# Kernel tuning notes

Hardware: AMD Instinct MI355X
Metric: run time of the kernel (lower is better)

## Reference

```python
import jax, jax.numpy as jnp
import numpy as np

T = 4096        # tokens
D = 1024        # input_dim
H = 2048        # expert_hidden_dim
O = 1024        # output_dim
E = 8           # num_experts
K = 2           # top_k


def setup_inputs() -> dict:
    key = jax.random.key(0)
    ks = jax.random.split(key, 7)
    s_in = 1.0 / np.sqrt(D)
    s_h = 1.0 / np.sqrt(H)
    return {
        "x": jax.random.normal(ks[0], (T, D), dtype=jnp.float32),
        "Wg": jax.random.uniform(ks[1], (D, E), jnp.float32, -s_in, s_in),
        "bg": jax.random.uniform(ks[2], (E,), jnp.float32, -s_in, s_in),
        "W1": jax.random.uniform(ks[3], (E, D, H), jnp.float32, -s_in, s_in),
        "b1": jax.random.uniform(ks[4], (E, H), jnp.float32, -s_in, s_in),
        "W2": jax.random.uniform(ks[5], (E, H, O), jnp.float32, -s_h, s_h),
        "b2": jax.random.uniform(ks[6], (E, O), jnp.float32, -s_h, s_h),
    }


def reference(x, Wg, bg, W1, b1, W2, b2):
    # Gating: top-k over expert logits, softmax over the k selected logits.
    logits = x @ Wg + bg                                  # [T, E]
    top_vals, top_idx = jax.lax.top_k(logits, K)          # [T, K]
    gates = jax.nn.softmax(top_vals, axis=-1)             # [T, K]

    # Expert MLPs (Linear -> ReLU -> Linear). Each token is processed by the
    # experts it routes to; since an expert's output on x is route-independent,
    # compute all expert outputs once and gather the selected ones (static
    # shapes, jit-friendly equivalent of the masked dispatch loop).
    h = jax.nn.relu(jnp.einsum('td,edh->eth', x, W1) + b1[:, None, :])  # [E,T,H]
    y = jnp.einsum('eth,eho->eto', h, W2) + b2[:, None, :]              # [E,T,O]

    sel = y[top_idx, jnp.arange(T)[:, None]]              # [T, K, O]
    # Weighted combine (scatter_add over batch_idx == per-token sum over K).
    return jnp.sum(sel * gates[..., None], axis=1)        # [T, O]
```

## Files before the change

kernel.cpp:

```cpp
#include <hip/hip_runtime.h>
#include <math.h>


#define T_TOK 4096
#define DIM   1024
#define HID   2048
#define OUTD  1024
#define NE    8

typedef __bf16 bf16_t;
typedef __bf16 bf16x8 __attribute__((ext_vector_type(8)));
typedef float  f32x4  __attribute__((ext_vector_type(4)));

typedef __attribute__((address_space(3))) void       as3_void;
typedef __attribute__((address_space(1))) const void as1_void;
#define GLDS16(src, dst) \
  __builtin_amdgcn_global_load_lds((as1_void*)(src), (as3_void*)(dst), 16, 0, 0)

#define FENCE() asm volatile("" ::: "memory")
#define BARRIER() do { FENCE(); __builtin_amdgcn_s_barrier(); FENCE(); } while (0)
#define LGKM_WAIT() do { \
    asm volatile("s_waitcnt lgkmcnt(0)" ::: "memory"); \
    __builtin_amdgcn_sched_barrier(0); } while (0)
#define VMW_RING() do { \
    if (wid < 4) asm volatile("s_waitcnt vmcnt(4)" ::: "memory"); \
    else         asm volatile("s_waitcnt vmcnt(3)" ::: "memory"); } while (0)
#define VM_WAIT0() asm volatile("s_waitcnt vmcnt(0)" ::: "memory")

__device__ __forceinline__ void gate_body(int bid, const float* __restrict__ x,
                                          const float* __restrict__ Wg,
                                          const float* __restrict__ bg,
                                          int* __restrict__ einfo,
                                          float2* __restrict__ gpair,
                                          bf16_t* __restrict__ xb) {
  int wid  = threadIdx.x >> 6;
  int lane = threadIdx.x & 63;
  int t = bid * 4 + wid;

  const float4* xr = (const float4*)(x + (size_t)t * DIM);
  float4 xv4[4];
  float sf[NE];
#pragma unroll
  for (int e = 0; e < NE; ++e) sf[e] = 0.f;

#pragma unroll
  for (int i = 0; i < 4; ++i) {
    int q = lane + 64 * i;
    float4 xv = xr[q];
    xv4[i] = xv;
    int d = q * 4;
#pragma unroll
    for (int c = 0; c < 4; ++c) {
      float xc = (&xv.x)[c];
      const float4* wr = (const float4*)(Wg + (size_t)(d + c) * NE);
      float4 w0 = wr[0], w1 = wr[1];
      sf[0] += xc * w0.x; sf[1] += xc * w0.y;
      sf[2] += xc * w0.z; sf[3] += xc * w0.w;
      sf[4] += xc * w1.x; sf[5] += xc * w1.y;
      sf[6] += xc * w1.z; sf[7] += xc * w1.w;
    }
  }

  ushort4* xbr = (ushort4*)(xb + (size_t)t * DIM);
#pragma unroll
  for (int i = 0; i < 4; ++i) {
    union { bf16_t b[4]; ushort4 u; } cv;
    cv.b[0] = (bf16_t)xv4[i].x; cv.b[1] = (bf16_t)xv4[i].y;
    cv.b[2] = (bf16_t)xv4[i].z; cv.b[3] = (bf16_t)xv4[i].w;
    xbr[lane + 64 * i] = cv.u;
  }

  double s[NE];
#pragma unroll
  for (int e = 0; e < NE; ++e) s[e] = (double)sf[e];
#pragma unroll
  for (int off = 32; off > 0; off >>= 1) {
#pragma unroll
    for (int e = 0; e < NE; ++e) s[e] += __shfl_xor(s[e], off);
  }

  if (lane == 0) {
    double v0 = -1e300, v1 = -1e300;
    int i0 = 0, i1 = 0;
#pragma unroll
    for (int e = 0; e < NE; ++e) {
      double v = s[e] + (double)bg[e];
      if (v > v0)      { v1 = v0; i1 = i0; v0 = v; i0 = e; }
      else if (v > v1) { v1 = v;  i1 = e; }
    }
    float ex = expf((float)(v1 - v0));
    float inv = 1.0f / (1.0f + ex);
    einfo[t] = i0 | (i1 << 8);
    gpair[t] = make_float2(inv, ex * inv);
  }
}

__device__ __forceinline__ void tr_body(const float* __restrict__ W,
                                        bf16_t* __restrict__ Wt, int R, int C,
                                        int bx, int by, int e, char* lds) {
  size_t ebase = (size_t)e * R * C;
  const int r0 = by * 64, c0 = bx * 128;
  const int tid = threadIdx.x;
#pragma unroll
  for (int it = 0; it < 8; ++it) {
    int f = tid + 256 * it;
    int row = f >> 5, cq = f & 31;
    float4 v = *(const float4*)&W[ebase + (size_t)(r0 + row) * C + c0 + cq * 4];
    union { bf16_t b[4]; unsigned long long u; } cv;
    cv.b[0] = (bf16_t)v.x; cv.b[1] = (bf16_t)v.y;
    cv.b[2] = (bf16_t)v.z; cv.b[3] = (bf16_t)v.w;
    *(unsigned long long*)(lds + row * 256 + ((cq ^ (row & 31)) << 3)) = cv.u;
  }
  __syncthreads();
#pragma unroll
  for (int p = 0; p < 4; ++p) {
    int q = tid + 256 * p;
    int orow = q >> 3, j = q & 7;
    union { bf16_t b[8]; uint4 u; } cv;
#pragma unroll
    for (int i = 0; i < 8; ++i) {
      int r = j * 8 + i;
      cv.b[i] = *(const bf16_t*)(lds + r * 256 +
                                 ((((orow >> 2) ^ (r & 31)) << 3) +
                                  ((orow & 3) << 1)));
    }
    *(uint4*)&Wt[ebase + (size_t)(c0 + orow) * R + r0 + j * 8] = cv.u;
  }
}

#define NB_GATE (T_TOK / 4)
#define NB_TR1  ((DIM / 64) * (HID / 128) * NE)
#define NB_TR2  ((HID / 64) * (OUTD / 128) * NE)
__global__ void k_front(const float* __restrict__ x, const float* __restrict__ Wg,
                        const float* __restrict__ bg, int* __restrict__ einfo,
                        float2* __restrict__ gpair, bf16_t* __restrict__ xb,
                        const float* __restrict__ W1, bf16_t* __restrict__ W1t,
                        const float* __restrict__ W2, bf16_t* __restrict__ W2t) {
  __shared__ __align__(16) char lds[16384];
  int bid = blockIdx.x;
  if (bid < NB_GATE) {
    gate_body(bid, x, Wg, bg, einfo, gpair, xb);
  } else if (bid < NB_GATE + NB_TR1) {
    int i = bid - NB_GATE;
    int nbx = HID / 128, nby = DIM / 64;
    tr_body(W1, W1t, DIM, HID, i % nbx, (i / nbx) % nby, i / (nbx * nby), lds);
  } else {
    int i = bid - NB_GATE - NB_TR1;
    int nbx = OUTD / 128, nby = HID / 64;
    tr_body(W2, W2t, HID, OUTD, i % nbx, (i / nbx) % nby, i / (nbx * nby), lds);
  }
}

__global__ void k_bin(const int* __restrict__ einfo, const float2* __restrict__ gpair,
                      int* __restrict__ cnt, int* __restrict__ offs,
                      int* __restrict__ elist, float* __restrict__ egate,
                      int* __restrict__ tokrec) {
  __shared__ int scnt[NE];
  int w = threadIdx.x >> 6;
  int lane = threadIdx.x & 63;
  unsigned long long below = (lane == 0) ? 0ull : ((~0ull) >> (64 - lane));
  int base = 0;
  for (int c = 0; c < T_TOK / 64; ++c) {
    int t = c * 64 + lane;
    int ei = einfo[t];
    float2 g = gpair[t];
    int e0 = ei & 0xff, e1 = ei >> 8;
    bool m0 = (e0 == w);
    bool m  = m0 || (e1 == w);
    unsigned long long mask = __ballot(m);
    if (m) {
      int pos = base + (int)__popcll(mask & below);
      elist[w * T_TOK + pos] = t;
      egate[w * T_TOK + pos] = m0 ? g.x : g.y;
      tokrec[2 * t + (m0 ? 0 : 1)] = (w << 16) | pos;
    }
    base += (int)__popcll(mask);
  }
  if (lane == 0) scnt[w] = base;
  __syncthreads();
  if (threadIdx.x == 0) {
    int a = 0;
#pragma unroll
    for (int e = 0; e < NE; ++e) {
      cnt[e] = scnt[e];
      offs[e] = a;
      a += scnt[e];
    }
    offs[NE] = a;
  }
}

#define STAGE_A(TT, HH) do { \
    char* _d = smem + (((TT) & 1) * 24576) + ((HH) * 12288); \
    GLDS16(Abase + offA[HH][0] + (TT) * 128, _d + tid * 16); \
    if (tid < 256) GLDS16(Abase + offA[HH][1] + (TT) * 128, _d + (512 + tid) * 16); \
  } while (0)

#define STAGE_B(TT, HH) do { \
    char* _d = smem + 49152 + (((TT) & 1) * 32768) + ((HH) * 16384); \
    GLDS16(Bbase + offB[HH][0] + (TT) * 128, _d + tid * 16); \
    GLDS16(Bbase + offB[HH][1] + (TT) * 128, _d + (512 + tid) * 16); \
  } while (0)

#define MFMA_Q(AF, BF, AH, BH) \
    _Pragma("unroll") for (int i = 0; i < 3; ++i) \
      _Pragma("unroll") for (int j = 0; j < 2; ++j) \
        _Pragma("unroll") for (int kk = 0; kk < 2; ++kk) \
          acc[(AH) * 3 + i][(BH) * 2 + j] = \
            __builtin_amdgcn_mfma_f32_16x16x32_bf16(AF[i][kk], BF[j][kk], \
                acc[(AH) * 3 + i][(BH) * 2 + j], 0, 0, 0)

#define RD_AF(SL) \
    _Pragma("unroll") for (int i = 0; i < 3; ++i) \
      _Pragma("unroll") for (int kk = 0; kk < 2; ++kk) \
        af[i][kk] = *(const bf16x8*)((SL) + rdA[i][kk])

#define KTILE(TT, NTc) do { \
    const char* _a0 = smem + (((TT) & 1) * 24576); \
    const char* _a1 = smem + (((TT) & 1) * 24576) + 12288; \
    const char* _b0 = smem + 49152 + (((TT) & 1) * 32768); \
    const char* _b1 = smem + 49152 + (((TT) & 1) * 32768) + 16384; \
    bf16x8 af[3][2], bf0[2][2], bf1[2][2]; \
    RD_AF(_a0); \
    _Pragma("unroll") for (int j = 0; j < 2; ++j) \
      _Pragma("unroll") for (int kk = 0; kk < 2; ++kk) { \
        bf0[j][kk] = *(const bf16x8*)(_b0 + rdB[j][kk]); \
        bf1[j][kk] = *(const bf16x8*)(_b1 + rdB[j][kk]); \
      } \
    if ((TT) + 1 < (NTc)) { STAGE_A((TT) + 1, 1); STAGE_B((TT) + 1, 1); } \
    BARRIER(); LGKM_WAIT(); \
    __builtin_amdgcn_s_setprio(1); \
    MFMA_Q(af, bf0, 0, 0); MFMA_Q(af, bf1, 0, 1); \
    __builtin_amdgcn_s_setprio(0); BARRIER(); \
    RD_AF(_a1); \
    if ((TT) + 2 < (NTc)) { STAGE_A((TT) + 2, 0); STAGE_B((TT) + 2, 0); \
      VMW_RING(); } \
    else { VM_WAIT0(); } \
    BARRIER(); LGKM_WAIT(); \
    __builtin_amdgcn_s_setprio(1); \
    MFMA_Q(af, bf0, 1, 0); MFMA_Q(af, bf1, 1, 1); \
    __builtin_amdgcn_s_setprio(0); BARRIER(); \
  } while (0)

__launch_bounds__(512, 2)
__global__ void k_gemm1(const bf16_t* __restrict__ xb, const bf16_t* __restrict__ W1t,
                        const float* __restrict__ b1, const int* __restrict__ cnt,
                        const int* __restrict__ offs, const int* __restrict__ elist,
                        bf16_t* __restrict__ hbuf) {
  const int e = blockIdx.z;
  const int count = cnt[e];
  const int rt = blockIdx.y;
  if (rt * 192 >= count) return;
  const int nt = blockIdx.x;

  __shared__ __align__(16) char smem[114688];

  const int tid = threadIdx.x, lane = tid & 63, wid = tid >> 6;
  const int wm = wid >> 2, wn = wid & 3;
  const int fr = lane & 15, lh = lane >> 4;

  unsigned offA[2][2], offB[2][2];
#pragma unroll
  for (int j = 0; j < 2; ++j) {
    int q = j * 512 + tid;
    int r = q >> 3, sfg = (q & 7) ^ (r & 7);
#pragma unroll
    for (int h = 0; h < 2; ++h) {
      int ar = r < 96 ? r : 95;
      int gr = rt * 192 + h * 96 + ar;
      if (gr > count - 1) gr = count - 1;
      int tok = elist[e * T_TOK + gr];
      offA[h][j] = (unsigned)((tok * DIM + sfg * 8) * 2);
      int brow = nt * 256 + h * 128 + r;
      offB[h][j] = (unsigned)(((e * HID + brow) * DIM + sfg * 8) * 2);
    }
  }
  unsigned rdA[3][2], rdB[2][2];
#pragma unroll
  for (int i = 0; i < 3; ++i) {
    int r = wm * 48 + i * 16 + fr;
#pragma unroll
    for (int kk = 0; kk < 2; ++kk)
      rdA[i][kk] = (unsigned)(r * 128 + (((kk * 4 + lh) ^ (r & 7)) * 16));
  }
#pragma unroll
  for (int j = 0; j < 2; ++j) {
    int r = wn * 32 + j * 16 + fr;
#pragma unroll
    for (int kk = 0; kk < 2; ++kk)
      rdB[j][kk] = (unsigned)(r * 128 + (((kk * 4 + lh) ^ (r & 7)) * 16));
  }

  const char* Abase = (const char*)xb;
  const char* Bbase = (const char*)W1t;

  f32x4 acc[6][4];
#pragma unroll
  for (int i = 0; i < 6; ++i)
#pragma unroll
    for (int j = 0; j < 4; ++j) acc[i][j] = (f32x4){0.f, 0.f, 0.f, 0.f};

  const int NT = DIM / 64;
  STAGE_A(0, 0); STAGE_B(0, 0); STAGE_A(0, 1); STAGE_B(0, 1);
  STAGE_A(1, 0); STAGE_B(1, 0);
  VMW_RING();
  BARRIER();

  for (int t = 0; t < NT; ++t) KTILE(t, NT);

  const int hbase = offs[e];
#pragma unroll
  for (int mi = 0; mi < 6; ++mi) {
#pragma unroll
    for (int rr = 0; rr < 4; ++rr) {
      int rowp = rt * 192 + (mi / 3) * 96 + wm * 48 + (mi % 3) * 16 + lh * 4 + rr;
      if (rowp < count) {
        size_t hrow = (size_t)(hbase + rowp) * HID;
#pragma unroll
        for (int nj = 0; nj < 4; ++nj) {
          int col = nt * 256 + (nj >> 1) * 128 + wn * 32 + (nj & 1) * 16 + fr;
          float v = acc[mi][nj][rr] + b1[e * HID + col];
          hbuf[hrow + col] = (bf16_t)(v > 0.f ? v : 0.f);
        }
      }
    }
  }
}

__launch_bounds__(512, 2)
__global__ void k_gemm2(const bf16_t* __restrict__ hbuf, const bf16_t* __restrict__ W2t,
                        const float* __restrict__ b2, const int* __restrict__ cnt,
                        const int* __restrict__ offs, const float* __restrict__ egate,
                        float* __restrict__ y) {
  const int e = blockIdx.z;
  const int count = cnt[e];
  const int rt = blockIdx.y;
  if (rt * 192 >= count) return;
  const int nt = blockIdx.x;

  __shared__ __align__(16) char smem[114688];

  const int tid = threadIdx.x, lane = tid & 63, wid = tid >> 6;
  const int wm = wid >> 2, wn = wid & 3;
  const int fr = lane & 15, lh = lane >> 4;
  const int hbase = offs[e];

  unsigned offA[2][2], offB[2][2];
#pragma unroll
  for (int j = 0; j < 2; ++j) {
    int q = j * 512 + tid;
    int r = q >> 3, sfg = (q & 7) ^ (r & 7);
#pragma unroll
    for (int h = 0; h < 2; ++h) {
      int ar = r < 96 ? r : 95;
      int gr = rt * 192 + h * 96 + ar;
      if (gr > count - 1) gr = count - 1;
      offA[h][j] = (unsigned)(((hbase + gr) * HID + sfg * 8) * 2);
      int brow = nt * 256 + h * 128 + r;
      offB[h][j] = (unsigned)(((e * OUTD + brow) * HID + sfg * 8) * 2);
    }
  }
  unsigned rdA[3][2], rdB[2][2];
#pragma unroll
  for (int i = 0; i < 3; ++i) {
    int r = wm * 48 + i * 16 + fr;
#pragma unroll
    for (int kk = 0; kk < 2; ++kk)
      rdA[i][kk] = (unsigned)(r * 128 + (((kk * 4 + lh) ^ (r & 7)) * 16));
  }
#pragma unroll
  for (int j = 0; j < 2; ++j) {
    int r = wn * 32 + j * 16 + fr;
#pragma unroll
    for (int kk = 0; kk < 2; ++kk)
      rdB[j][kk] = (unsigned)(r * 128 + (((kk * 4 + lh) ^ (r & 7)) * 16));
  }

  const char* Abase = (const char*)hbuf;
  const char* Bbase = (const char*)W2t;

  f32x4 acc[6][4];
#pragma unroll
  for (int i = 0; i < 6; ++i)
#pragma unroll
    for (int j = 0; j < 4; ++j) acc[i][j] = (f32x4){0.f, 0.f, 0.f, 0.f};

  const int NT = HID / 64;
  STAGE_A(0, 0); STAGE_B(0, 0); STAGE_A(0, 1); STAGE_B(0, 1);
  STAGE_A(1, 0); STAGE_B(1, 0);
  VMW_RING();
  BARRIER();

  for (int t = 0; t < NT; ++t) KTILE(t, NT);

#pragma unroll
  for (int mi = 0; mi < 6; ++mi) {
#pragma unroll
    for (int rr = 0; rr < 4; ++rr) {
      int rowp = rt * 192 + (mi / 3) * 96 + wm * 48 + (mi % 3) * 16 + lh * 4 + rr;
      if (rowp < count) {
        float gate = egate[e * T_TOK + rowp];
        size_t yrow = (size_t)(hbase + rowp) * OUTD;
#pragma unroll
        for (int nj = 0; nj < 4; ++nj) {
          int col = nt * 256 + (nj >> 1) * 128 + wn * 32 + (nj & 1) * 16 + fr;
          y[yrow + col] = gate * (acc[mi][nj][rr] + b2[e * OUTD + col]);
        }
      }
    }
  }
}

__global__ void k_combine(const float* __restrict__ y, const int* __restrict__ offs,
                          const int* __restrict__ tokrec, float* __restrict__ out) {
  int t = blockIdx.x;
  int r0 = tokrec[2 * t], r1 = tokrec[2 * t + 1];
  int s0 = offs[r0 >> 16] + (r0 & 0xffff);
  int s1 = offs[r1 >> 16] + (r1 & 0xffff);
  const float4* ya = (const float4*)(y + (size_t)s0 * OUTD);
  const float4* yb = (const float4*)(y + (size_t)s1 * OUTD);
  float4* o = (float4*)(out + (size_t)t * OUTD);
  int i = threadIdx.x;
  float4 a = ya[i], b = yb[i];
  o[i] = make_float4(a.x + b.x, a.y + b.y, a.z + b.z, a.w + b.w);
}

extern "C" void kernel_launch(void* const* d_in, const int* in_sizes, int n_in,
                              void* d_out, int out_size, void* d_ws, size_t ws_size,
                              hipStream_t stream) {
  const float* x  = (const float*)d_in[0];
  const float* Wg = (const float*)d_in[1];
  const float* bg = (const float*)d_in[2];
  const float* W1 = (const float*)d_in[3];
  const float* b1 = (const float*)d_in[4];
  const float* W2 = (const float*)d_in[5];
  const float* b2 = (const float*)d_in[6];
  float* out = (float*)d_out;

  char* ws = (char*)d_ws;
  int*    cnt    = (int*)(ws);
  int*    offs   = (int*)(ws + 1024);
  int*    tokrec = (int*)(ws + 4096);
  int*    einfo  = (int*)(ws + 36864);
  float2* gpair  = (float2*)(ws + 53248);
  int*    elist  = (int*)(ws + 131072);
  float*  egate  = (float*)(ws + 262144);
  bf16_t* W1t    = (bf16_t*)(ws + (1u << 20));
  float*  y      = (float*)(ws + (1u << 20));
  bf16_t* W2t    = (bf16_t*)(ws + (1u << 20) + (32u << 20));
  bf16_t* xb     = (bf16_t*)(ws + (1u << 20) + (64u << 20));
  bf16_t* hbuf   = (bf16_t*)(ws + (1u << 20) + (72u << 20));

  k_front<<<NB_GATE + NB_TR1 + NB_TR2, 256, 0, stream>>>(
      x, Wg, bg, einfo, gpair, xb, W1, W1t, W2, W2t);
  k_bin<<<1, 512, 0, stream>>>(einfo, gpair, cnt, offs, elist, egate, tokrec);

  k_gemm1<<<dim3(HID / 256, 22, NE), 512, 0, stream>>>(
      xb, W1t, b1, cnt, offs, elist, hbuf);
  k_gemm2<<<dim3(OUTD / 256, 22, NE), 512, 0, stream>>>(
      hbuf, W2t, b2, cnt, offs, egate, y);
  k_combine<<<T_TOK, 256, 0, stream>>>(y, offs, tokrec, out);
}
```

Measured before the change: 200.5 us.

## Move W2 transpose-convert into extra gemm1 grid slice to overlap with GEMM

The fp32-to-bf16 transpose of W2 is removed from the front kernel and performed by an extra z-slice of the gemm1 grid (176 blocks, each handling two tiles per iteration with split LDS halves). The aim is to shorten the front kernel and overlap the W2 conversion with the first expert GEMM, filling CUs left idle by early-exiting row tiles. The cost is that these conversion blocks compete with gemm1 blocks for CU slots, memory bandwidth and a large LDS allocation. tr_body also gains an extra barrier.

```diff
diff --git a/kernel.cpp b/kernel.cpp
--- a/kernel.cpp
+++ b/kernel.cpp
@@ -97,57 +97,57 @@
 
 __device__ __forceinline__ void tr_body(const float* __restrict__ W,
                                         bf16_t* __restrict__ Wt, int R, int C,
-                                        int bx, int by, int e, char* lds) {
+                                        int bx, int by, int e, char* lds,
+                                        int tid, bool valid) {
   size_t ebase = (size_t)e * R * C;
   const int r0 = by * 64, c0 = bx * 128;
-  const int tid = threadIdx.x;
-#pragma unroll
-  for (int it = 0; it < 8; ++it) {
-    int f = tid + 256 * it;
-    int row = f >> 5, cq = f & 31;
-    float4 v = *(const float4*)&W[ebase + (size_t)(r0 + row) * C + c0 + cq * 4];
-    union { bf16_t b[4]; unsigned long long u; } cv;
-    cv.b[0] = (bf16_t)v.x; cv.b[1] = (bf16_t)v.y;
-    cv.b[2] = (bf16_t)v.z; cv.b[3] = (bf16_t)v.w;
-    *(unsigned long long*)(lds + row * 256 + ((cq ^ (row & 31)) << 3)) = cv.u;
+  if (valid) {
+#pragma unroll
+    for (int it = 0; it < 8; ++it) {
+      int f = tid + 256 * it;
+      int row = f >> 5, cq = f & 31;
+      float4 v = *(const float4*)&W[ebase + (size_t)(r0 + row) * C + c0 + cq * 4];
+      union { bf16_t b[4]; unsigned long long u; } cv;
+      cv.b[0] = (bf16_t)v.x; cv.b[1] = (bf16_t)v.y;
+      cv.b[2] = (bf16_t)v.z; cv.b[3] = (bf16_t)v.w;
+      *(unsigned long long*)(lds + row * 256 + ((cq ^ (row & 31)) << 3)) = cv.u;
+    }
   }
   __syncthreads();
-#pragma unroll
-  for (int p = 0; p < 4; ++p) {
-    int q = tid + 256 * p;
-    int orow = q >> 3, j = q & 7;
-    union { bf16_t b[8]; uint4 u; } cv;
-#pragma unroll
-    for (int i = 0; i < 8; ++i) {
-      int r = j * 8 + i;
-      cv.b[i] = *(const bf16_t*)(lds + r * 256 +
-                                 ((((orow >> 2) ^ (r & 31)) << 3) +
-                                  ((orow & 3) << 1)));
-    }
-    *(uint4*)&Wt[ebase + (size_t)(c0 + orow) * R + r0 + j * 8] = cv.u;
-  }
+  if (valid) {
+#pragma unroll
+    for (int p = 0; p < 4; ++p) {
+      int q = tid + 256 * p;
+      int orow = q >> 3, j = q & 7;
+      union { bf16_t b[8]; uint4 u; } cv;
+#pragma unroll
+      for (int i = 0; i < 8; ++i) {
+        int r = j * 8 + i;
+        cv.b[i] = *(const bf16_t*)(lds + r * 256 +
+                                   ((((orow >> 2) ^ (r & 31)) << 3) +
+                                    ((orow & 3) << 1)));
+      }
+      *(uint4*)&Wt[ebase + (size_t)(c0 + orow) * R + r0 + j * 8] = cv.u;
+    }
+  }
+  __syncthreads();
 }
 
 #define NB_GATE (T_TOK / 4)
 #define NB_TR1  ((DIM / 64) * (HID / 128) * NE)
-#define NB_TR2  ((HID / 64) * (OUTD / 128) * NE)
 __global__ void k_front(const float* __restrict__ x, const float* __restrict__ Wg,
                         const float* __restrict__ bg, int* __restrict__ einfo,
                         float2* __restrict__ gpair, bf16_t* __restrict__ xb,
-                        const float* __restrict__ W1, bf16_t* __restrict__ W1t,
-                        const float* __restrict__ W2, bf16_t* __restrict__ W2t) {
+                        const float* __restrict__ W1, bf16_t* __restrict__ W1t) {
   __shared__ __align__(16) char lds[16384];
   int bid = blockIdx.x;
   if (bid < NB_GATE) {
     gate_body(bid, x, Wg, bg, einfo, gpair, xb);
-  } else if (bid < NB_GATE + NB_TR1) {
+  } else {
     int i = bid - NB_GATE;
     int nbx = HID / 128, nby = DIM / 64;
-    tr_body(W1, W1t, DIM, HID, i % nbx, (i / nbx) % nby, i / (nbx * nby), lds);
-  } else {
-    int i = bid - NB_GATE - NB_TR1;
-    int nbx = OUTD / 128, nby = HID / 64;
-    tr_body(W2, W2t, HID, OUTD, i % nbx, (i / nbx) % nby, i / (nbx * nby), lds);
+    tr_body(W1, W1t, DIM, HID, i % nbx, (i / nbx) % nby, i / (nbx * nby),
+            lds, threadIdx.x, true);
   }
 }
 
@@ -246,16 +246,35 @@
 __global__ void k_gemm1(const bf16_t* __restrict__ xb, const bf16_t* __restrict__ W1t,
                         const float* __restrict__ b1, const int* __restrict__ cnt,
                         const int* __restrict__ offs, const int* __restrict__ elist,
-                        bf16_t* __restrict__ hbuf) {
+                        bf16_t* __restrict__ hbuf,
+                        const float* __restrict__ W2, bf16_t* __restrict__ W2t) {
+  __shared__ __align__(16) char smem[114688];
+  const int tid = threadIdx.x;
+
+  if (blockIdx.z == NE) {
+    int bid2 = blockIdx.y * (HID / 256) + blockIdx.x;
+    char* lds2 = smem + ((tid >= 256) ? 16384 : 0);
+    int ltid = tid & 255;
+    const int NTILE = (HID / 64) * (OUTD / 128) * NE;
+    int nbx = OUTD / 128, nby = HID / 64;
+    for (int it = 0; it < 6; ++it) {
+      int tile = it * 352 + bid2 * 2 + (tid >= 256 ? 1 : 0);
+      bool valid = tile < NTILE;
+      int bx = valid ? tile % nbx : 0;
+      int by = valid ? (tile / nbx) % nby : 0;
+      int e2 = valid ? tile / (nbx * nby) : 0;
+      tr_body(W2, W2t, HID, OUTD, bx, by, e2, lds2, ltid, valid);
+    }
+    return;
+  }
+
   const int e = blockIdx.z;
   const int count = cnt[e];
   const int rt = blockIdx.y;
   if (rt * 192 >= count) return;
   const int nt = blockIdx.x;
 
-  __shared__ __align__(16) char smem[114688];
-
-  const int tid = threadIdx.x, lane = tid & 63, wid = tid >> 6;
+  const int lane = tid & 63, wid = tid >> 6;
   const int wm = wid >> 2, wn = wid & 3;
   const int fr = lane & 15, lh = lane >> 4;
 
@@ -451,12 +470,12 @@
   bf16_t* xb     = (bf16_t*)(ws + (1u << 20) + (64u << 20));
   bf16_t* hbuf   = (bf16_t*)(ws + (1u << 20) + (72u << 20));
 
-  k_front<<<NB_GATE + NB_TR1 + NB_TR2, 256, 0, stream>>>(
-      x, Wg, bg, einfo, gpair, xb, W1, W1t, W2, W2t);
+  k_front<<<NB_GATE + NB_TR1, 256, 0, stream>>>(
+      x, Wg, bg, einfo, gpair, xb, W1, W1t);
   k_bin<<<1, 512, 0, stream>>>(einfo, gpair, cnt, offs, elist, egate, tokrec);
 
-  k_gemm1<<<dim3(HID / 256, 22, NE), 512, 0, stream>>>(
-      xb, W1t, b1, cnt, offs, elist, hbuf);
+  k_gemm1<<<dim3(HID / 256, 22, NE + 1), 512, 0, stream>>>(
+      xb, W1t, b1, cnt, offs, elist, hbuf, W2, W2t);
   k_gemm2<<<dim3(OUTD / 256, 22, NE), 512, 0, stream>>>(
       hbuf, W2t, b2, cnt, offs, egate, y);
   k_combine<<<T_TOK, 256, 0, stream>>>(y, offs, tokrec, out);
```

Measured after the change: 202.3 us. No clear change (+0.9%).
